# Kernel optimization log

Hardware: AMD Instinct MI355X
Metric: run time of the kernel (lower is better)

The kernel has to match this reference:

```python
import jax, jax.numpy as jnp
import numpy as np
from jax import lax

ALPHA = 0.1  # leak rate dt/tau
T, B, NIN, N, NOUT = 1024, 64, 32, 256, 16


def setup_inputs() -> dict:
    key = jax.random.key(0)
    ks = jax.random.split(key, 6)
    inputs = jax.random.normal(ks[0], (T, B, NIN), dtype=jnp.float32)
    noise = jax.random.normal(ks[1], (T, B, N), dtype=jnp.float32)
    x0 = jax.random.normal(ks[2], (B, N), dtype=jnp.float32)
    Win = jax.random.normal(ks[3], (NIN, N), dtype=jnp.float32) / np.sqrt(NIN)
    Wrec = jax.random.normal(ks[4], (N, N), dtype=jnp.float32) / np.sqrt(N)
    brec = jnp.zeros((N,), dtype=jnp.float32)
    Wout = jax.random.normal(ks[5], (N, NOUT), dtype=jnp.float32) / np.sqrt(N)
    bout = jnp.zeros((NOUT,), dtype=jnp.float32)
    return {"inputs": inputs, "noise": noise, "x0": x0, "Win": Win,
            "Wrec": Wrec, "brec": brec, "Wout": Wout, "bout": bout}


def reference(inputs, noise, x0, Win, Wrec, brec, Wout, bout):
    """Leaky vanilla RNN over T steps.
    x_t = (1-a)*x_{t-1} + a*(u_t@Win + tanh(x_{t-1})@Wrec + brec) + q_t
    z_t = tanh(x_t)@Wout + bout
    Returns (outputs [T,B,Nout], states [T,B,N]).
    """
    def step(x_tm1, uq):
        u_t, q_t = uq
        r_tm1 = jnp.tanh(x_tm1)
        x_t = (1.0 - ALPHA) * x_tm1 + ALPHA * (
            u_t @ Win + r_tm1 @ Wrec + brec) + q_t
        z_t = jnp.tanh(x_t) @ Wout + bout
        return x_t, (z_t, x_t)

    _, (outputs, states) = lax.scan(step, x0, (inputs, noise))
    return outputs, states
```

## Files before the change

kernel.cpp:

```cpp
#include <hip/hip_runtime.h>

#define T_STEPS 1024
#define BATCH   64
#define NIN     32
#define NH      256
#define NOUT    16

typedef __attribute__((ext_vector_type(8))) _Float16 half8;
typedef __attribute__((ext_vector_type(4))) _Float16 half4;
typedef __attribute__((ext_vector_type(4))) float    f32x4;

__device__ __forceinline__ float fast_tanh(float x) {
  float e = __builtin_amdgcn_exp2f(x * 2.8853900817779268f);
  return 1.0f - 2.0f * __builtin_amdgcn_rcpf(e + 1.0f);
}

#define ROW 320
#define BUFSZ (16 * 320)


__global__ __launch_bounds__(256, 2)
void RecurrentNetwork_19628000543215_ukernel(
    const float* __restrict__ inputs,
    const float* __restrict__ noise,
    const float* __restrict__ Win,
    const float* __restrict__ brec,
    float* __restrict__ U)
{
  const int tid = threadIdx.x;
  const int wv  = tid >> 6;
  const int l   = tid & 63;
  const int m   = l & 15;
  const int q   = l >> 4;

  half8 wf[16];
  f32x4 bs[16];
  #pragma unroll
  for (int nt = 0; nt < 16; ++nt) {
    #pragma unroll
    for (int j = 0; j < 8; ++j)
      wf[nt][j] = (_Float16)(0.1f * Win[(size_t)(8 * q + j) * NH + 16 * nt + m]);
    bs[nt] = 0.1f * (*(const f32x4*)(brec + 16 * nt + 4 * q));
  }

  #pragma unroll
  for (int s = 0; s < 2; ++s) {
    const int tile = blockIdx.x * 4 + wv + s * 2048;
    const int row  = tile * 16 + m;
    const float* up = inputs + (size_t)row * NIN + 8 * q;
    const f32x4 ua = *(const f32x4*)up;
    const f32x4 ub = *(const f32x4*)(up + 4);
    half8 uf;
    uf[0]=(_Float16)ua.x; uf[1]=(_Float16)ua.y; uf[2]=(_Float16)ua.z; uf[3]=(_Float16)ua.w;
    uf[4]=(_Float16)ub.x; uf[5]=(_Float16)ub.y; uf[6]=(_Float16)ub.z; uf[7]=(_Float16)ub.w;

    const float* qp = noise + (size_t)row * NH;
    float*       Up = U     + (size_t)row * NH;
    #pragma unroll
    for (int nt = 0; nt < 16; ++nt) {
      f32x4 acc = bs[nt] + *(const f32x4*)(qp + 16 * nt + 4 * q);
      acc = __builtin_amdgcn_mfma_f32_16x16x32_f16(wf[nt], uf, acc, 0, 0, 0);
      *(f32x4*)(Up + 16 * nt + 4 * q) = acc;
    }
  }
}

__global__ __launch_bounds__(512, 2)
void RecurrentNetwork_19628000543215_kernel(
    const float* __restrict__ Uu,
    const float* __restrict__ x0,
    const float* __restrict__ Wrec,
    float* __restrict__ outx)
{
  __shared__ alignas(16) unsigned short rlds[2 * BUFSZ];

  const int g   = blockIdx.x;
  const int tid = threadIdx.x;
  const int w   = tid >> 6;
  const int l   = tid & 63;
  const int m   = l & 15;
  const int q   = l >> 4;
  const int b   = 16 * g + m;
  const int mx  = m & 7;

  half8 wr[2][8];
  int   ldso[8];
  #pragma unroll
  for (int i = 0; i < 8; ++i) {
    const int kt = (w + i) & 7;
    ldso[i] = m * ROW + ((((4 * kt + q) ^ mx)) << 3);
    #pragma unroll
    for (int nt = 0; nt < 2; ++nt) {
      const int n = 32 * w + 16 * nt + m;
      #pragma unroll
      for (int j = 0; j < 8; ++j) {
        const int k = 32 * kt + 8 * q + j;
        wr[nt][i][j] = (_Float16)(0.1f * Wrec[(size_t)k * NH + n]);
      }
    }
  }

  f32x4 x[2];
  #pragma unroll
  for (int nt = 0; nt < 2; ++nt)
    x[nt] = *(const f32x4*)(x0 + (size_t)b * NH + 32 * w + 16 * nt + 4 * q);

  #pragma unroll
  for (int nt = 0; nt < 2; ++nt) {
    const int n0 = 32 * w + 16 * nt + 4 * q;
    half4 r;
    r.x = (_Float16)fast_tanh(x[nt].x);
    r.y = (_Float16)fast_tanh(x[nt].y);
    r.z = (_Float16)fast_tanh(x[nt].z);
    r.w = (_Float16)fast_tanh(x[nt].w);
    const int blk = (n0 >> 3) ^ mx;
    *(half4*)&rlds[m * ROW + blk * 8 + (n0 & 7)] = r;
  }
  f32x4 qv[2];
  qv[0] = *(const f32x4*)(Uu + (size_t)b * NH + 32 * w + 4 * q);
  qv[1] = *(const f32x4*)(Uu + (size_t)b * NH + 32 * w + 16 + 4 * q);
  __syncthreads();

  half8 bfw = *(const half8*)&rlds[ldso[0]];

  const float* np = Uu   + (size_t)BATCH * NH + (size_t)b * NH + 32 * w + 4 * q;
  float*       xp = outx + (size_t)b * NH + 32 * w + 4 * q;

  #pragma unroll 1
  for (int t = 0; t < T_STEPS; ++t) {
    const int rb = (t & 1) * BUFSZ;
    const int wb = BUFSZ - rb;

    const f32x4 qn0 = *(const f32x4*)np;
    const f32x4 qn1 = *(const f32x4*)(np + 16);

    f32x4 accA[2], accB[2];
    accA[0] = qv[0]; accA[1] = qv[1];
    accB[0] = f32x4{0.f, 0.f, 0.f, 0.f};
    accB[1] = f32x4{0.f, 0.f, 0.f, 0.f};

    accA[0] = __builtin_amdgcn_mfma_f32_16x16x32_f16(wr[0][0], bfw, accA[0], 0, 0, 0);
    accA[1] = __builtin_amdgcn_mfma_f32_16x16x32_f16(wr[1][0], bfw, accA[1], 0, 0, 0);
    #pragma unroll
    for (int i = 1; i < 8; ++i) {
      const half8 bf = *(const half8*)&rlds[rb + ldso[i]];
      if (i & 1) {
        accB[0] = __builtin_amdgcn_mfma_f32_16x16x32_f16(wr[0][i], bf, accB[0], 0, 0, 0);
        accB[1] = __builtin_amdgcn_mfma_f32_16x16x32_f16(wr[1][i], bf, accB[1], 0, 0, 0);
      } else {
        accA[0] = __builtin_amdgcn_mfma_f32_16x16x32_f16(wr[0][i], bf, accA[0], 0, 0, 0);
        accA[1] = __builtin_amdgcn_mfma_f32_16x16x32_f16(wr[1][i], bf, accA[1], 0, 0, 0);
      }
    }

    x[0] = 0.9f * x[0] + (accA[0] + accB[0]);
    x[1] = 0.9f * x[1] + (accA[1] + accB[1]);

    #pragma unroll
    for (int nt = 0; nt < 2; ++nt) {
      const int n0 = 32 * w + 16 * nt + 4 * q;
      half4 r;
      auto plo = __builtin_amdgcn_cvt_pkrtz(fast_tanh(x[nt].x), fast_tanh(x[nt].y));
      auto phi = __builtin_amdgcn_cvt_pkrtz(fast_tanh(x[nt].z), fast_tanh(x[nt].w));
      r.x = plo.x; r.y = plo.y; r.z = phi.x; r.w = phi.y;
      const int blk = (n0 >> 3) ^ mx;
      *(half4*)&rlds[wb + m * ROW + blk * 8 + (n0 & 7)] = r;
    }

    asm volatile("" ::: "memory");
    bfw = *(const half8*)&rlds[wb + ldso[0]];

    *(f32x4*)(xp)      = x[0];
    *(f32x4*)(xp + 16) = x[1];
    qv[0] = qn0; qv[1] = qn1;
    const bool adv = (t <= T_STEPS - 3);
    np += adv ? (size_t)(BATCH * NH) : (size_t)0;
    xp += (size_t)(BATCH * NH);

    asm volatile("s_waitcnt lgkmcnt(0)" ::: "memory");
    __builtin_amdgcn_s_barrier();
    asm volatile("" ::: "memory");
  }
}

__global__ __launch_bounds__(256, 4)
void RecurrentNetwork_19628000543215_zkernel(
    const float* __restrict__ states,
    const float* __restrict__ Wout,
    const float* __restrict__ bout,
    float* __restrict__ outz)
{
  const int tid  = threadIdx.x;
  const int wv   = tid >> 6;
  const int l    = tid & 63;
  const int m    = l & 15;
  const int q    = l >> 4;
  const int tile = blockIdx.x * 4 + wv;
  const int row  = tile * 16 + m;

  half8 wo[8];
  #pragma unroll
  for (int kt = 0; kt < 8; ++kt)
    #pragma unroll
    for (int j = 0; j < 8; ++j)
      wo[kt][j] = (_Float16)Wout[(size_t)(32 * kt + 8 * q + j) * NOUT + m];

  f32x4 zac = *(const f32x4*)(bout + 4 * q);
  const float* xrow = states + (size_t)row * NH;

  #pragma unroll
  for (int kt = 0; kt < 8; ++kt) {
    const f32x4 xa = *(const f32x4*)(xrow + 32 * kt + 8 * q);
    const f32x4 xb = *(const f32x4*)(xrow + 32 * kt + 8 * q + 4);
    half8 rf;
    rf[0] = (_Float16)fast_tanh(xa.x);
    rf[1] = (_Float16)fast_tanh(xa.y);
    rf[2] = (_Float16)fast_tanh(xa.z);
    rf[3] = (_Float16)fast_tanh(xa.w);
    rf[4] = (_Float16)fast_tanh(xb.x);
    rf[5] = (_Float16)fast_tanh(xb.y);
    rf[6] = (_Float16)fast_tanh(xb.z);
    rf[7] = (_Float16)fast_tanh(xb.w);
    zac = __builtin_amdgcn_mfma_f32_16x16x32_f16(wo[kt], rf, zac, 0, 0, 0);
  }
  *(f32x4*)(outz + (size_t)row * NOUT + 4 * q) = zac;
}

extern "C" void kernel_launch(void* const* d_in, const int* in_sizes, int n_in,
                              void* d_out, int out_size, void* d_ws, size_t ws_size,
                              hipStream_t stream) {
  (void)in_sizes; (void)n_in; (void)out_size; (void)d_ws; (void)ws_size;
  float* outz = (float*)d_out;
  float* outx = (float*)d_out + (size_t)T_STEPS * BATCH * NOUT;
  RecurrentNetwork_19628000543215_ukernel<<<dim3(512), dim3(256), 0, stream>>>(
      (const float*)d_in[0],
      (const float*)d_in[1],
      (const float*)d_in[3],
      (const float*)d_in[5],
      outx);
  RecurrentNetwork_19628000543215_kernel<<<dim3(4), dim3(512), 0, stream>>>(
      outx,
      (const float*)d_in[2],
      (const float*)d_in[4],
      outx);
  RecurrentNetwork_19628000543215_zkernel<<<dim3(1024), dim3(256), 0, stream>>>(
      outx,
      (const float*)d_in[6],
      (const float*)d_in[7],
      outz);
}
```

Measured before the change: 1.095 ms.

## Permute Wrec K-order so each lane writes its own tanh fragment directly

Reorders the K index within each 32-wide chunk of the recurrent weights so that the eight hidden values a lane produces (two 4-wide groups) form exactly its own MFMA B fragment. The lane then keeps that fragment in registers instead of reading it back from LDS after the write, and the two half4 stores become one half8 store. The time loop is also unrolled by two so buffer offsets are constants, and all seven LDS reads are issued before the MFMAs. The aim is to shorten the serial per-step critical path (one LDS round trip fewer plus address arithmetic), at the cost of more registers and a more delicate index mapping.

```diff
diff --git a/kernel.cpp b/kernel.cpp
--- a/kernel.cpp
+++ b/kernel.cpp
@@ -7,7 +7,6 @@
 #define NOUT    16
 
 typedef __attribute__((ext_vector_type(8))) _Float16 half8;
-typedef __attribute__((ext_vector_type(4))) _Float16 half4;
 typedef __attribute__((ext_vector_type(4))) float    f32x4;
 
 __device__ __forceinline__ float fast_tanh(float x) {
@@ -15,8 +14,8 @@
   return 1.0f - 2.0f * __builtin_amdgcn_rcpf(e + 1.0f);
 }
 
-#define ROW 320
-#define BUFSZ (16 * 320)
+#define ROWB 640
+#define BUFB (16 * 640)
 
 
 __global__ __launch_bounds__(256, 2)
@@ -72,7 +71,7 @@
     const float* __restrict__ Wrec,
     float* __restrict__ outx)
 {
-  __shared__ alignas(16) unsigned short rlds[2 * BUFSZ];
+  __shared__ alignas(16) char rlds[2 * BUFB];
 
   const int g   = blockIdx.x;
   const int tid = threadIdx.x;
@@ -88,99 +87,103 @@
   #pragma unroll
   for (int i = 0; i < 8; ++i) {
     const int kt = (w + i) & 7;
-    ldso[i] = m * ROW + ((((4 * kt + q) ^ mx)) << 3);
+    ldso[i] = m * ROWB + (((4 * kt + q) ^ mx) << 4);
     #pragma unroll
     for (int nt = 0; nt < 2; ++nt) {
       const int n = 32 * w + 16 * nt + m;
       #pragma unroll
       for (int j = 0; j < 8; ++j) {
-        const int k = 32 * kt + 8 * q + j;
-        wr[nt][i][j] = (_Float16)(0.1f * Wrec[(size_t)k * NH + n]);
+        const int kk = 32 * kt + (j < 4 ? 4 * q + j : 16 + 4 * q + (j - 4));
+        wr[nt][i][j] = (_Float16)(0.1f * Wrec[(size_t)kk * NH + n]);
       }
     }
   }
 
   f32x4 x[2];
-  #pragma unroll
-  for (int nt = 0; nt < 2; ++nt)
-    x[nt] = *(const f32x4*)(x0 + (size_t)b * NH + 32 * w + 16 * nt + 4 * q);
-
-  #pragma unroll
-  for (int nt = 0; nt < 2; ++nt) {
-    const int n0 = 32 * w + 16 * nt + 4 * q;
-    half4 r;
-    r.x = (_Float16)fast_tanh(x[nt].x);
-    r.y = (_Float16)fast_tanh(x[nt].y);
-    r.z = (_Float16)fast_tanh(x[nt].z);
-    r.w = (_Float16)fast_tanh(x[nt].w);
-    const int blk = (n0 >> 3) ^ mx;
-    *(half4*)&rlds[m * ROW + blk * 8 + (n0 & 7)] = r;
+  x[0] = *(const f32x4*)(x0 + (size_t)b * NH + 32 * w + 4 * q);
+  x[1] = *(const f32x4*)(x0 + (size_t)b * NH + 32 * w + 16 + 4 * q);
+
+  half8 bfw;
+  {
+    const auto c0 = __builtin_amdgcn_cvt_pkrtz(fast_tanh(x[0].x), fast_tanh(x[0].y));
+    const auto c1 = __builtin_amdgcn_cvt_pkrtz(fast_tanh(x[0].z), fast_tanh(x[0].w));
+    const auto c2 = __builtin_amdgcn_cvt_pkrtz(fast_tanh(x[1].x), fast_tanh(x[1].y));
+    const auto c3 = __builtin_amdgcn_cvt_pkrtz(fast_tanh(x[1].z), fast_tanh(x[1].w));
+    half8 r;
+    r[0]=(_Float16)c0.x; r[1]=(_Float16)c0.y; r[2]=(_Float16)c1.x; r[3]=(_Float16)c1.y;
+    r[4]=(_Float16)c2.x; r[5]=(_Float16)c2.y; r[6]=(_Float16)c3.x; r[7]=(_Float16)c3.y;
+    *(half8*)(rlds + ldso[0]) = r;
+    bfw = r;
   }
   f32x4 qv[2];
   qv[0] = *(const f32x4*)(Uu + (size_t)b * NH + 32 * w + 4 * q);
   qv[1] = *(const f32x4*)(Uu + (size_t)b * NH + 32 * w + 16 + 4 * q);
   __syncthreads();
 
-  half8 bfw = *(const half8*)&rlds[ldso[0]];
-
   const float* np = Uu   + (size_t)BATCH * NH + (size_t)b * NH + 32 * w + 4 * q;
   float*       xp = outx + (size_t)b * NH + 32 * w + 4 * q;
 
+#define RNN_STEP(RB, WB, TCUR)                                               \
+  {                                                                          \
+    const f32x4 qn0 = *(const f32x4*)np;                                     \
+    const f32x4 qn1 = *(const f32x4*)(np + 16);                              \
+    const half8 bf1 = *(const half8*)(rlds + (RB) + ldso[1]);                \
+    const half8 bf2 = *(const half8*)(rlds + (RB) + ldso[2]);                \
+    const half8 bf3 = *(const half8*)(rlds + (RB) + ldso[3]);                \
+    const half8 bf4 = *(const half8*)(rlds + (RB) + ldso[4]);                \
+    const half8 bf5 = *(const half8*)(rlds + (RB) + ldso[5]);                \
+    const half8 bf6 = *(const half8*)(rlds + (RB) + ldso[6]);                \
+    const half8 bf7 = *(const half8*)(rlds + (RB) + ldso[7]);                \
+    f32x4 accA0 = qv[0], accA1 = qv[1];                                      \
+    f32x4 accB0 = f32x4{0.f,0.f,0.f,0.f}, accB1 = f32x4{0.f,0.f,0.f,0.f};    \
+    accA0 = __builtin_amdgcn_mfma_f32_16x16x32_f16(wr[0][0], bfw, accA0, 0, 0, 0); \
+    accA1 = __builtin_amdgcn_mfma_f32_16x16x32_f16(wr[1][0], bfw, accA1, 0, 0, 0); \
+    accB0 = __builtin_amdgcn_mfma_f32_16x16x32_f16(wr[0][1], bf1, accB0, 0, 0, 0); \
+    accB1 = __builtin_amdgcn_mfma_f32_16x16x32_f16(wr[1][1], bf1, accB1, 0, 0, 0); \
+    accA0 = __builtin_amdgcn_mfma_f32_16x16x32_f16(wr[0][2], bf2, accA0, 0, 0, 0); \
+    accA1 = __builtin_amdgcn_mfma_f32_16x16x32_f16(wr[1][2], bf2, accA1, 0, 0, 0); \
+    accB0 = __builtin_amdgcn_mfma_f32_16x16x32_f16(wr[0][3], bf3, accB0, 0, 0, 0); \
+    accB1 = __builtin_amdgcn_mfma_f32_16x16x32_f16(wr[1][3], bf3, accB1, 0, 0, 0); \
+    accA0 = __builtin_amdgcn_mfma_f32_16x16x32_f16(wr[0][4], bf4, accA0, 0, 0, 0); \
+    accA1 = __builtin_amdgcn_mfma_f32_16x16x32_f16(wr[1][4], bf4, accA1, 0, 0, 0); \
+    accB0 = __builtin_amdgcn_mfma_f32_16x16x32_f16(wr[0][5], bf5, accB0, 0, 0, 0); \
+    accB1 = __builtin_amdgcn_mfma_f32_16x16x32_f16(wr[1][5], bf5, accB1, 0, 0, 0); \
+    accA0 = __builtin_amdgcn_mfma_f32_16x16x32_f16(wr[0][6], bf6, accA0, 0, 0, 0); \
+    accA1 = __builtin_amdgcn_mfma_f32_16x16x32_f16(wr[1][6], bf6, accA1, 0, 0, 0); \
+    accB0 = __builtin_amdgcn_mfma_f32_16x16x32_f16(wr[0][7], bf7, accB0, 0, 0, 0); \
+    accB1 = __builtin_amdgcn_mfma_f32_16x16x32_f16(wr[1][7], bf7, accB1, 0, 0, 0); \
+    x[0] = 0.9f * x[0] + (accA0 + accB0);                                    \
+    x[1] = 0.9f * x[1] + (accA1 + accB1);                                    \
+    {                                                                        \
+      const auto c0 = __builtin_amdgcn_cvt_pkrtz(fast_tanh(x[0].x), fast_tanh(x[0].y)); \
+      const auto c1 = __builtin_amdgcn_cvt_pkrtz(fast_tanh(x[0].z), fast_tanh(x[0].w)); \
+      const auto c2 = __builtin_amdgcn_cvt_pkrtz(fast_tanh(x[1].x), fast_tanh(x[1].y)); \
+      const auto c3 = __builtin_amdgcn_cvt_pkrtz(fast_tanh(x[1].z), fast_tanh(x[1].w)); \
+      half8 r;                                                               \
+      r[0]=(_Float16)c0.x; r[1]=(_Float16)c0.y;                              \
+      r[2]=(_Float16)c1.x; r[3]=(_Float16)c1.y;                              \
+      r[4]=(_Float16)c2.x; r[5]=(_Float16)c2.y;                              \
+      r[6]=(_Float16)c3.x; r[7]=(_Float16)c3.y;                              \
+      *(half8*)(rlds + (WB) + ldso[0]) = r;                                  \
+      bfw = r;                                                               \
+    }                                                                        \
+    *(f32x4*)(xp)      = x[0];                                               \
+    *(f32x4*)(xp + 16) = x[1];                                               \
+    qv[0] = qn0; qv[1] = qn1;                                                \
+    const bool adv = ((TCUR) <= T_STEPS - 3);                                \
+    np += adv ? (size_t)(BATCH * NH) : (size_t)0;                            \
+    xp += (size_t)(BATCH * NH);                                              \
+    asm volatile("s_waitcnt lgkmcnt(0)" ::: "memory");                       \
+    __builtin_amdgcn_s_barrier();                                            \
+    asm volatile("" ::: "memory");                                           \
+  }
+
   #pragma unroll 1
-  for (int t = 0; t < T_STEPS; ++t) {
-    const int rb = (t & 1) * BUFSZ;
-    const int wb = BUFSZ - rb;
-
-    const f32x4 qn0 = *(const f32x4*)np;
-    const f32x4 qn1 = *(const f32x4*)(np + 16);
-
-    f32x4 accA[2], accB[2];
-    accA[0] = qv[0]; accA[1] = qv[1];
-    accB[0] = f32x4{0.f, 0.f, 0.f, 0.f};
-    accB[1] = f32x4{0.f, 0.f, 0.f, 0.f};
-
-    accA[0] = __builtin_amdgcn_mfma_f32_16x16x32_f16(wr[0][0], bfw, accA[0], 0, 0, 0);
-    accA[1] = __builtin_amdgcn_mfma_f32_16x16x32_f16(wr[1][0], bfw, accA[1], 0, 0, 0);
-    #pragma unroll
-    for (int i = 1; i < 8; ++i) {
-      const half8 bf = *(const half8*)&rlds[rb + ldso[i]];
-      if (i & 1) {
-        accB[0] = __builtin_amdgcn_mfma_f32_16x16x32_f16(wr[0][i], bf, accB[0], 0, 0, 0);
-        accB[1] = __builtin_amdgcn_mfma_f32_16x16x32_f16(wr[1][i], bf, accB[1], 0, 0, 0);
-      } else {
-        accA[0] = __builtin_amdgcn_mfma_f32_16x16x32_f16(wr[0][i], bf, accA[0], 0, 0, 0);
-        accA[1] = __builtin_amdgcn_mfma_f32_16x16x32_f16(wr[1][i], bf, accA[1], 0, 0, 0);
-      }
-    }
-
-    x[0] = 0.9f * x[0] + (accA[0] + accB[0]);
-    x[1] = 0.9f * x[1] + (accA[1] + accB[1]);
-
-    #pragma unroll
-    for (int nt = 0; nt < 2; ++nt) {
-      const int n0 = 32 * w + 16 * nt + 4 * q;
-      half4 r;
-      auto plo = __builtin_amdgcn_cvt_pkrtz(fast_tanh(x[nt].x), fast_tanh(x[nt].y));
-      auto phi = __builtin_amdgcn_cvt_pkrtz(fast_tanh(x[nt].z), fast_tanh(x[nt].w));
-      r.x = plo.x; r.y = plo.y; r.z = phi.x; r.w = phi.y;
-      const int blk = (n0 >> 3) ^ mx;
-      *(half4*)&rlds[wb + m * ROW + blk * 8 + (n0 & 7)] = r;
-    }
-
-    asm volatile("" ::: "memory");
-    bfw = *(const half8*)&rlds[wb + ldso[0]];
-
-    *(f32x4*)(xp)      = x[0];
-    *(f32x4*)(xp + 16) = x[1];
-    qv[0] = qn0; qv[1] = qn1;
-    const bool adv = (t <= T_STEPS - 3);
-    np += adv ? (size_t)(BATCH * NH) : (size_t)0;
-    xp += (size_t)(BATCH * NH);
-
-    asm volatile("s_waitcnt lgkmcnt(0)" ::: "memory");
-    __builtin_amdgcn_s_barrier();
-    asm volatile("" ::: "memory");
-  }
+  for (int t = 0; t < T_STEPS; t += 2) {
+    RNN_STEP(0,    BUFB, t)
+    RNN_STEP(BUFB, 0,    t + 1)
+  }
+#undef RNN_STEP
 }
 
 __global__ __launch_bounds__(256, 4)
```

After: 945.6 us. 1.16x faster.
